# Kernel optimization log

Hardware: AMD Instinct MI355X
Metric: run time of the kernel (lower is better)

The kernel has to match this reference:

```python
import jax, jax.numpy as jnp
import numpy as np

B, N, KNN_K, T_FRAC = 8, 4096, 32, 0.5
C_IN, C_OUT = 4, 64


def _knn_group(q, db, kk):
    """q: [Nq,3] queries, db: [Nd,3] database. Returns feats [Nq,kk,4], nn [Nq,kk,3]."""
    d2 = (jnp.sum(q * q, axis=-1, keepdims=True)
          + jnp.sum(db * db, axis=-1)[None, :]
          - 2.0 * (q @ db.T))                      # [Nq,Nd] squared dists
    _, idx = jax.lax.top_k(-d2, kk)                 # ascending distance, like pytorch3d knn_points
    nn = db[idx]                                    # [Nq,kk,3]
    resi = nn - q[:, None, :]                       # [Nq,kk,3]
    sq = jnp.sum(resi * resi, axis=-1, keepdims=True)
    dist = jnp.where(sq > 0, jnp.sqrt(jnp.where(sq > 0, sq, 1.0)), 0.0)  # safe norm (exact fwd)
    feats = jnp.concatenate([resi, dist], axis=-1)  # [Nq,kk,4]
    return feats, nn


def _forward(points1, points2, pc, Wq, Wk, Wv, bq, bk, bv, ridx1, ridx2, k, t):
    k2 = int(k * t)
    k1 = k - k2
    p1 = jnp.swapaxes(points1, 1, 2)  # [B,N,3]
    p2 = jnp.swapaxes(points2, 1, 2)
    p3 = jnp.swapaxes(pc, 1, 2)

    def per_batch(a, b, c, i1, i2):
        newp = jnp.concatenate([a[i1], b[i2]], axis=0)     # [N,3] fused candidate set
        f1, g1 = _knn_group(newp, a, k1)
        f2, g2 = _knn_group(newp, b, k2)
        f3, g3 = _knn_group(newp, c, k)
        feats = jnp.concatenate([f1, f2, f3], axis=1)      # [N,2k,4]
        grouped = jnp.concatenate([g1, g2, g3], axis=1)    # [N,2k,3]
        return feats, grouped

    feats, grouped = jax.vmap(per_batch)(p1, p2, p3, ridx1, ridx2)  # [B,N,2k,4], [B,N,2k,3]

    # SelfAttention over the neighbor axis (per point group)
    q = feats @ Wq + bq          # [B,N,2k,C_OUT]
    kf = feats @ Wk + bk
    v = feats @ Wv + bv
    scale = 1.0 / np.sqrt(C_OUT).astype(np.float32)
    attn = jax.nn.softmax(jnp.einsum('bnkc,bnjc->bnkj', q, kf) * scale, axis=-1)
    y = jnp.einsum('bnkj,bnjc->bnkc', attn, v)             # [B,N,2k,C_OUT]

    score = jnp.max(y, axis=-1)                            # max over channels -> [B,N,2k]
    w = jax.nn.softmax(score, axis=-1)                     # weights over 2k neighbors
    fused = jnp.einsum('bnk,bnkd->bdn', w, grouped)        # [B,3,N]
    return fused


def setup_inputs() -> dict:
    key = jax.random.key(0)
    ks = jax.random.split(key, 8)
    points1 = jax.random.normal(ks[0], (B, 3, N), dtype=jnp.float32)
    points2 = jax.random.normal(ks[1], (B, 3, N), dtype=jnp.float32)
    pc = jax.random.normal(ks[2], (B, 3, N), dtype=jnp.float32)
    N2 = int(N * T_FRAC)
    N1 = N - N2
    perm = lambda kk: jax.random.permutation(kk, N)
    ridx1 = jax.vmap(perm)(jax.random.split(ks[3], B))[:, :N1].astype(jnp.int32)
    ridx2 = jax.vmap(perm)(jax.random.split(ks[4], B))[:, :N2].astype(jnp.int32)
    s = 1.0 / np.sqrt(C_IN)
    Wq = jax.random.normal(ks[5], (C_IN, C_OUT), dtype=jnp.float32) * s
    Wk = jax.random.normal(ks[6], (C_IN, C_OUT), dtype=jnp.float32) * s
    Wv = jax.random.normal(ks[7], (C_IN, C_OUT), dtype=jnp.float32) * s
    z = jnp.zeros((C_OUT,), dtype=jnp.float32)
    return {"points1": points1, "points2": points2, "pc": pc,
            "Wq": Wq, "Wk": Wk, "Wv": Wv, "bq": z, "bk": z, "bv": z,
            "ridx1": ridx1, "ridx2": ridx2, "k": KNN_K, "t": T_FRAC}


def reference(points1, points2, pc, Wq, Wk, Wv, bq, bk, bv, ridx1, ridx2, k, t):
    return _forward(points1, points2, pc, Wq, Wk, Wv, bq, bk, bv, ridx1, ridx2, k, t)
```

## Files before the change

kernel.cpp:

```cpp
#include <hip/hip_runtime.h>
#include <hip/hip_bf16.h>
#include <math.h>

#define NB   8
#define NPT  4096
#define NQ1  2048
#define NQ2  2048
#define KTOT 64
#define TILE 1024
#define NTHR 256
#define QPB  128
#define TBUF 16
#define MPAD 33

#define RCPLN2 1.4426950408889634f
#define EXP2F(x) __builtin_amdgcn_exp2f(x)

#define PRM_OFF  (4u << 20)
#define PACK_OFF ((4u << 20) + 4096)

__global__ __launch_bounds__(256) void pf2_pack(const float* __restrict__ p1,
                                                const float* __restrict__ p2,
                                                const float* __restrict__ pc,
                                                float4* __restrict__ packed) {
    int t = blockIdx.x * 256 + threadIdx.x;
    int b = t / (3 * NPT);
    int r = t - b * 3 * NPT;
    int db = r / NPT;
    int j = r - db * NPT;
    const float* src = (db == 0 ? p1 : db == 1 ? p2 : pc) + (size_t)b * 3 * NPT;
    packed[t] = make_float4(src[j], src[NPT + j], src[2 * NPT + j], 0.f);
}

__global__ void pf2_setup(const float* __restrict__ Wq, const float* __restrict__ Wk,
                          const float* __restrict__ bq, const float* __restrict__ bk,
                          float* __restrict__ prm) {
    int t = threadIdx.x;
    const float sc = 0.125f * RCPLN2;
    if (t < 16) {
        int p = t >> 2, q = t & 3;
        float a = 0.f;
        for (int c = 0; c < 64; ++c) a += Wq[p * 64 + c] * Wk[q * 64 + c];
        prm[t] = a * sc;
    } else if (t < 20) {
        int p = t - 16; float a = 0.f;
        for (int c = 0; c < 64; ++c) a += Wq[p * 64 + c] * bk[c];
        prm[t] = a * sc;
    } else if (t < 24) {
        int q = t - 20; float a = 0.f;
        for (int c = 0; c < 64; ++c) a += Wk[q * 64 + c] * bq[c];
        prm[t] = a * sc;
    } else if (t == 24) {
        float a = 0.f;
        for (int c = 0; c < 64; ++c) a += bq[c] * bk[c];
        prm[t] = a * sc;
    }
}

template <int K>
__device__ __forceinline__ void insert_med3(float (&dl)[K], int (&il)[K], float d, int id) {
    float pd = -INFINITY; int pi = 0;
    bool cp = false;
#pragma unroll
    for (int j = 0; j < K; ++j) {
        float oj = dl[j]; int ij = il[j];
        bool cj = d < oj;
        dl[j] = __builtin_amdgcn_fmed3f(d, pd, oj);
        il[j] = cp ? pi : (cj ? id : ij);
        pd = oj; pi = ij; cp = cj;
    }
}

template <int K>
__device__ void knn_half(const float* __restrict__ dbp,
                         float qx, float qy, float qz, int tid,
                         float4* __restrict__ tileLds,
                         unsigned short* __restrict__ bufLds,
                         float* __restrict__ mD,
                         unsigned short* __restrict__ mI,
                         unsigned short* __restrict__ outIdx) {
    const int q = tid & (QPB - 1), h = tid >> 7;
    float dl[K]; int il[K];
#pragma unroll
    for (int j = 0; j < K; ++j) { dl[j] = INFINITY; il[j] = 0; }
    float thresh = INFINITY;
    int cnt = 0;
    float4* tp = tileLds + h * TILE;

    for (int st = 0; st < 2; ++st) {
        int base = h * 2048 + st * TILE;
        __syncthreads();
        for (int r = 0; r < TILE / QPB; ++r) {
            int j = q + r * QPB;
            float x = dbp[base + j];
            float y = dbp[NPT + base + j];
            float z = dbp[2 * NPT + base + j];
            tp[j] = make_float4(-2.f * x, -2.f * y, -2.f * z,
                                fmaf(x, x, fmaf(y, y, z * z)));
        }
        __syncthreads();

        for (int c0 = 0; c0 < TILE; c0 += 8) {
            float sv[8];
#pragma unroll
            for (int u = 0; u < 8; ++u) {
                float4 p = tp[c0 + u];
                sv[u] = fmaf(p.x, qx, fmaf(p.y, qy, fmaf(p.z, qz, p.w)));
            }
#pragma unroll
            for (int u = 0; u < 8; ++u) {
                if (sv[u] < thresh) {
                    bufLds[cnt * NTHR + tid] = (unsigned short)(c0 + u);
                    ++cnt;
                }
            }
            if (__any(cnt > TBUF - 8)) {
                for (int u = 0; u < TBUF; ++u) {
                    if (!__any(u < cnt)) break;
                    bool act = (u < cnt);
                    int j = act ? bufLds[u * NTHR + tid] : 0;
                    float4 p = tp[j];
                    float s = fmaf(p.x, qx, fmaf(p.y, qy, fmaf(p.z, qz, p.w)));
                    bool pass = act && (s < dl[K - 1]);
                    if (__any(pass)) {
                        if (pass) insert_med3<K>(dl, il, s, base + j);
                    }
                }
                cnt = 0;
                thresh = dl[K - 1];
            }
        }
        for (int u = 0; u < TBUF; ++u) {
            if (!__any(u < cnt)) break;
            bool act = (u < cnt);
            int j = act ? bufLds[u * NTHR + tid] : 0;
            float4 p = tp[j];
            float s = fmaf(p.x, qx, fmaf(p.y, qy, fmaf(p.z, qz, p.w)));
            bool pass = act && (s < dl[K - 1]);
            if (__any(pass)) {
                if (pass) insert_med3<K>(dl, il, s, base + j);
            }
        }
        cnt = 0;
        thresh = dl[K - 1];
    }

    __syncthreads();
    if (h == 1) {
#pragma unroll
        for (int j = 0; j < K; ++j) {
            mD[q * MPAD + j] = dl[j];
            mI[q * MPAD + j] = (unsigned short)il[j];
        }
    }
    __syncthreads();
    if (h == 0) {
#pragma unroll
        for (int j = 0; j < K; ++j) {
            float d = mD[q * MPAD + j];
            int id = (int)mI[q * MPAD + j];
            if (d < dl[K - 1]) insert_med3<K>(dl, il, d, id);
        }
        unsigned* o32 = (unsigned*)outIdx;
#pragma unroll
        for (int u = 0; u < K / 2; ++u)
            o32[u] = (unsigned)(unsigned short)il[2 * u] |
                     ((unsigned)(unsigned short)il[2 * u + 1] << 16);
    }
}

__global__ __launch_bounds__(NTHR) void pf2_knn(const float* __restrict__ p1,
                                                const float* __restrict__ p2,
                                                const float* __restrict__ pc,
                                                const int* __restrict__ ridx1,
                                                const int* __restrict__ ridx2,
                                                unsigned short* __restrict__ wsIdx) {
    __shared__ float4 tileLds[2 * TILE];
    __shared__ unsigned short bufLds[TBUF * NTHR];
    float* mD = (float*)tileLds;
    unsigned short* mI = (unsigned short*)(mD + QPB * MPAD);

    int bid = blockIdx.x;
    int dbslot = bid >> 8;
    int db = (dbslot == 0) ? 2 : dbslot - 1;
    int rem = bid & 255;
    int b = rem >> 5;
    int chunk = rem & 31;
    int tid = threadIdx.x;
    int i = chunk * QPB + (tid & (QPB - 1));

    int j0; const float* srcp;
    if (i < NQ1) { j0 = ridx1[b * NQ1 + i]; srcp = p1; }
    else         { j0 = ridx2[b * NQ2 + (i - NQ1)]; srcp = p2; }
    const float* sb = srcp + (size_t)b * 3 * NPT;
    float qx = sb[j0], qy = sb[NPT + j0], qz = sb[2 * NPT + j0];

    const float* dbp = (db == 0 ? p1 : db == 1 ? p2 : pc) + (size_t)b * 3 * NPT;
    unsigned short* out = wsIdx + (size_t)(b * NPT + i) * KTOT +
                          (db == 0 ? 0 : db == 1 ? 16 : 32);
    if (db < 2) knn_half<16>(dbp, qx, qy, qz, tid, tileLds, bufLds, mD, mI, out);
    else        knn_half<32>(dbp, qx, qy, qz, tid, tileLds, bufLds, mD, mI, out);
}

__global__ __launch_bounds__(256) void pf2_attn(const float* __restrict__ p1,
                                                const float* __restrict__ p2,
                                                const float* __restrict__ pc,
                                                const int* __restrict__ ridx1,
                                                const int* __restrict__ ridx2,
                                                const float* __restrict__ Wv,
                                                const float* __restrict__ bv,
                                                const float* __restrict__ prm,
                                                const float4* __restrict__ packed,
                                                const unsigned short* __restrict__ wsIdx,
                                                float* __restrict__ out) {
    __shared__ float4 wvt[64];
    __shared__ float  bvs[64];
    __shared__ float  prms[25];
    __shared__ float4 gl[4][64];
    __shared__ float4 fl[4][64];
    __shared__ float  sl[4][64];

    int tid = threadIdx.x;
    if (tid < 64) {
        wvt[tid] = make_float4(Wv[tid], Wv[64 + tid], Wv[128 + tid], Wv[192 + tid]);
        bvs[tid] = bv[tid];
    } else if (tid < 89) {
        prms[tid - 64] = prm[tid - 64];
    }
    __syncthreads();

    int wv = tid >> 6, lane = tid & 63;
    int g = blockIdx.x * 4 + wv;
    int b = g >> 12;
    int i = g & 4095;

    int j0; const float* srcp;
    if (i < NQ1) { j0 = ridx1[b * NQ1 + i]; srcp = p1; }
    else         { j0 = ridx2[b * NQ2 + (i - NQ1)]; srcp = p2; }
    const float* sb = srcp + (size_t)b * 3 * NPT;
    float qx = sb[j0], qy = sb[NPT + j0], qz = sb[2 * NPT + j0];

    int nidx = (int)wsIdx[(size_t)(b * NPT + i) * KTOT + lane];
    int db = (lane < 16) ? 0 : (lane < 32) ? 1 : 2;
    float4 np = packed[(size_t)(b * 3 + db) * NPT + nidx];
    float nx = np.x, ny = np.y, nz = np.z;
    float fx = nx - qx, fy = ny - qy, fz = nz - qz;
    float sq = fx * fx + fy * fy + fz * fz;
    float fw = sq > 0.f ? sqrtf(sq) : 0.f;

    float gx = prms[0]  * fx + prms[1]  * fy + prms[2]  * fz + prms[3]  * fw;
    float gy = prms[4]  * fx + prms[5]  * fy + prms[6]  * fz + prms[7]  * fw;
    float gz = prms[8]  * fx + prms[9]  * fy + prms[10] * fz + prms[11] * fw;
    float gw = prms[12] * fx + prms[13] * fy + prms[14] * fz + prms[15] * fw;
    float sj = prms[20] * fx + prms[21] * fy + prms[22] * fz + prms[23] * fw;

    gl[wv][lane] = make_float4(gx, gy, gz, gw);
    fl[wv][lane] = make_float4(fx, fy, fz, fw);
    sl[wv][lane] = sj;
    __syncthreads();

    float m = -INFINITY;
    for (int j = 0; j < 64; ++j) {
        float4 gj = gl[wv][j];
        float l = fx * gj.x + fy * gj.y + fz * gj.z + fw * gj.w + sl[wv][j];
        m = fmaxf(m, l);
    }
    float S = 0.f, H0 = 0.f, H1 = 0.f, H2 = 0.f, H3 = 0.f;
    for (int j = 0; j < 64; ++j) {
        float4 gj = gl[wv][j];
        float4 fj = fl[wv][j];
        float l = fx * gj.x + fy * gj.y + fz * gj.z + fw * gj.w + sl[wv][j];
        float e = EXP2F(l - m);
        S += e;
        H0 += e * fj.x; H1 += e * fj.y; H2 += e * fj.z; H3 += e * fj.w;
    }
    float rS = 1.f / S;

    float smax = -INFINITY;
    for (int ch = 0; ch < 64; ++ch) {
        float4 wc = wvt[ch];
        float t = H0 * wc.x + H1 * wc.y + H2 * wc.z + H3 * wc.w;
        float yv = fmaf(t, rS, bvs[ch]);
        smax = fmaxf(smax, yv);
    }

    float M = smax;
    for (int off = 32; off; off >>= 1) M = fmaxf(M, __shfl_xor(M, off));
    float e = EXP2F((smax - M) * RCPLN2);
    float E = e;
    for (int off = 32; off; off >>= 1) E += __shfl_xor(E, off);
    float w = e / E;
    float px = w * nx, py = w * ny, pz = w * nz;
    for (int off = 32; off; off >>= 1) {
        px += __shfl_xor(px, off);
        py += __shfl_xor(py, off);
        pz += __shfl_xor(pz, off);
    }
    if (lane == 0) {
        float* ob = out + (size_t)b * 3 * NPT + i;
        ob[0] = px; ob[NPT] = py; ob[2 * NPT] = pz;
    }
}

extern "C" void kernel_launch(void* const* d_in, const int* in_sizes, int n_in,
                              void* d_out, int out_size, void* d_ws, size_t ws_size,
                              hipStream_t stream) {
    const float* p1 = (const float*)d_in[0];
    const float* p2 = (const float*)d_in[1];
    const float* pc = (const float*)d_in[2];
    const float* Wq = (const float*)d_in[3];
    const float* Wk = (const float*)d_in[4];
    const float* Wv = (const float*)d_in[5];
    const float* bq = (const float*)d_in[6];
    const float* bk = (const float*)d_in[7];
    const float* bv = (const float*)d_in[8];
    const int* ridx1 = (const int*)d_in[9];
    const int* ridx2 = (const int*)d_in[10];
    float* out = (float*)d_out;

    unsigned short* wsIdx = (unsigned short*)d_ws;
    float* prm = (float*)((char*)d_ws + PRM_OFF);
    float4* packed = (float4*)((char*)d_ws + PACK_OFF);

    pf2_pack<<<(3 * NB * NPT) / 256, 256, 0, stream>>>(p1, p2, pc, packed);
    pf2_setup<<<1, 32, 0, stream>>>(Wq, Wk, bq, bk, prm);
    pf2_knn<<<NB * 3 * (NPT / QPB), NTHR, 0, stream>>>(p1, p2, pc, ridx1, ridx2, wsIdx);
    pf2_attn<<<NB * NPT / 4, 256, 0, stream>>>(p1, p2, pc, ridx1, ridx2, Wv, bv, prm,
                                               packed, wsIdx, out);
}
```

Baseline: 378.4 us.

## Two-pass KNN: distance-only top-K threshold then index selection over full LDS tile

The KNN selection is split into two passes. The first keeps only sorted distances, buffering raw distance values so candidates need no recompute and no index bookkeeping, and yields the exact K-th distance. The second rescans with that threshold and inserts indices for only the few survivors. The whole 4096-point database is now staged once into LDS (64KB tile, larger buffer of 32-bit entries), which removes the per-subtile reload syncs but doubles the distance computation and raises LDS use, which may lower occupancy.

```diff
diff --git a/kernel.cpp b/kernel.cpp
--- a/kernel.cpp
+++ b/kernel.cpp
@@ -7,7 +7,6 @@
 #define NQ1  2048
 #define NQ2  2048
 #define KTOT 64
-#define TILE 1024
 #define NTHR 256
 #define QPB  128
 #define TBUF 16
@@ -72,84 +71,100 @@
 }
 
 template <int K>
-__device__ void knn_half(const float* __restrict__ dbp,
-                         float qx, float qy, float qz, int tid,
-                         float4* __restrict__ tileLds,
-                         unsigned short* __restrict__ bufLds,
+__device__ void knn_half(float qx, float qy, float qz, int tid,
+                         const float4* __restrict__ tile,
+                         unsigned* __restrict__ dbuf,
                          float* __restrict__ mD,
                          unsigned short* __restrict__ mI,
                          unsigned short* __restrict__ outIdx) {
     const int q = tid & (QPB - 1), h = tid >> 7;
-    float dl[K]; int il[K];
-#pragma unroll
-    for (int j = 0; j < K; ++j) { dl[j] = INFINITY; il[j] = 0; }
+    const int base = h * 2048;
+
+    float dl[K];
+#pragma unroll
+    for (int j = 0; j < K; ++j) dl[j] = INFINITY;
     float thresh = INFINITY;
     int cnt = 0;
-    float4* tp = tileLds + h * TILE;
-
-    for (int st = 0; st < 2; ++st) {
-        int base = h * 2048 + st * TILE;
-        __syncthreads();
-        for (int r = 0; r < TILE / QPB; ++r) {
-            int j = q + r * QPB;
-            float x = dbp[base + j];
-            float y = dbp[NPT + base + j];
-            float z = dbp[2 * NPT + base + j];
-            tp[j] = make_float4(-2.f * x, -2.f * y, -2.f * z,
-                                fmaf(x, x, fmaf(y, y, z * z)));
-        }
-        __syncthreads();
-
-        for (int c0 = 0; c0 < TILE; c0 += 8) {
-            float sv[8];
-#pragma unroll
-            for (int u = 0; u < 8; ++u) {
-                float4 p = tp[c0 + u];
-                sv[u] = fmaf(p.x, qx, fmaf(p.y, qy, fmaf(p.z, qz, p.w)));
+
+    auto flushD = [&]() {
+        for (int u = 0; u < TBUF; ++u) {
+            if (!__any(u < cnt)) break;
+            unsigned bits = dbuf[u * NTHR + tid];
+            float s = (u < cnt) ? __uint_as_float(bits) : INFINITY;
+            float pd = -INFINITY;
+#pragma unroll
+            for (int j = 0; j < K; ++j) {
+                float oj = dl[j];
+                dl[j] = __builtin_amdgcn_fmed3f(s, pd, oj);
+                pd = oj;
             }
-#pragma unroll
-            for (int u = 0; u < 8; ++u) {
-                if (sv[u] < thresh) {
-                    bufLds[cnt * NTHR + tid] = (unsigned short)(c0 + u);
-                    ++cnt;
-                }
+        }
+        cnt = 0;
+        thresh = dl[K - 1];
+    };
+
+    for (int c0 = 0; c0 < 2048; c0 += 8) {
+        float sv[8];
+#pragma unroll
+        for (int u = 0; u < 8; ++u) {
+            float4 p = tile[base + c0 + u];
+            sv[u] = fmaf(p.x, qx, fmaf(p.y, qy, fmaf(p.z, qz, p.w)));
+        }
+#pragma unroll
+        for (int u = 0; u < 8; ++u) {
+            if (sv[u] < thresh) {
+                dbuf[cnt * NTHR + tid] = __float_as_uint(sv[u]);
+                ++cnt;
             }
-            if (__any(cnt > TBUF - 8)) {
-                for (int u = 0; u < TBUF; ++u) {
-                    if (!__any(u < cnt)) break;
-                    bool act = (u < cnt);
-                    int j = act ? bufLds[u * NTHR + tid] : 0;
-                    float4 p = tp[j];
-                    float s = fmaf(p.x, qx, fmaf(p.y, qy, fmaf(p.z, qz, p.w)));
-                    bool pass = act && (s < dl[K - 1]);
-                    if (__any(pass)) {
-                        if (pass) insert_med3<K>(dl, il, s, base + j);
-                    }
-                }
-                cnt = 0;
-                thresh = dl[K - 1];
-            }
-        }
+        }
+        if (__any(cnt > TBUF - 8)) flushD();
+    }
+    flushD();
+    const float mt = dl[K - 1];
+
+    int il[K]; float dl2[K];
+#pragma unroll
+    for (int j = 0; j < K; ++j) { dl2[j] = INFINITY; il[j] = 0; }
+    cnt = 0;
+
+    auto flushI = [&]() {
         for (int u = 0; u < TBUF; ++u) {
             if (!__any(u < cnt)) break;
             bool act = (u < cnt);
-            int j = act ? bufLds[u * NTHR + tid] : 0;
-            float4 p = tp[j];
+            int idx = act ? (int)dbuf[u * NTHR + tid] : 0;
+            float4 p = tile[idx];
             float s = fmaf(p.x, qx, fmaf(p.y, qy, fmaf(p.z, qz, p.w)));
-            bool pass = act && (s < dl[K - 1]);
+            bool pass = act && (s < dl2[K - 1]);
             if (__any(pass)) {
-                if (pass) insert_med3<K>(dl, il, s, base + j);
+                if (pass) insert_med3<K>(dl2, il, s, idx);
             }
         }
         cnt = 0;
-        thresh = dl[K - 1];
-    }
+    };
+
+    for (int c0 = 0; c0 < 2048; c0 += 8) {
+        float sv[8];
+#pragma unroll
+        for (int u = 0; u < 8; ++u) {
+            float4 p = tile[base + c0 + u];
+            sv[u] = fmaf(p.x, qx, fmaf(p.y, qy, fmaf(p.z, qz, p.w)));
+        }
+#pragma unroll
+        for (int u = 0; u < 8; ++u) {
+            if (sv[u] <= mt) {
+                dbuf[cnt * NTHR + tid] = (unsigned)(base + c0 + u);
+                ++cnt;
+            }
+        }
+        if (__any(cnt > TBUF - 8)) flushI();
+    }
+    flushI();
 
     __syncthreads();
     if (h == 1) {
 #pragma unroll
         for (int j = 0; j < K; ++j) {
-            mD[q * MPAD + j] = dl[j];
+            mD[q * MPAD + j] = dl2[j];
             mI[q * MPAD + j] = (unsigned short)il[j];
         }
     }
@@ -159,7 +174,7 @@
         for (int j = 0; j < K; ++j) {
             float d = mD[q * MPAD + j];
             int id = (int)mI[q * MPAD + j];
-            if (d < dl[K - 1]) insert_med3<K>(dl, il, d, id);
+            if (d < dl2[K - 1]) insert_med3<K>(dl2, il, d, id);
         }
         unsigned* o32 = (unsigned*)outIdx;
 #pragma unroll
@@ -175,8 +190,8 @@
                                                 const int* __restrict__ ridx1,
                                                 const int* __restrict__ ridx2,
                                                 unsigned short* __restrict__ wsIdx) {
-    __shared__ float4 tileLds[2 * TILE];
-    __shared__ unsigned short bufLds[TBUF * NTHR];
+    __shared__ float4 tileLds[NPT];
+    __shared__ unsigned dbuf[TBUF * NTHR];
     float* mD = (float*)tileLds;
     unsigned short* mI = (unsigned short*)(mD + QPB * MPAD);
 
@@ -196,10 +211,21 @@
     float qx = sb[j0], qy = sb[NPT + j0], qz = sb[2 * NPT + j0];
 
     const float* dbp = (db == 0 ? p1 : db == 1 ? p2 : pc) + (size_t)b * 3 * NPT;
+
+    for (int r = 0; r < NPT / NTHR; ++r) {
+        int j = tid + r * NTHR;
+        float x = dbp[j];
+        float y = dbp[NPT + j];
+        float z = dbp[2 * NPT + j];
+        tileLds[j] = make_float4(-2.f * x, -2.f * y, -2.f * z,
+                                 fmaf(x, x, fmaf(y, y, z * z)));
+    }
+    __syncthreads();
+
     unsigned short* out = wsIdx + (size_t)(b * NPT + i) * KTOT +
                           (db == 0 ? 0 : db == 1 ? 16 : 32);
-    if (db < 2) knn_half<16>(dbp, qx, qy, qz, tid, tileLds, bufLds, mD, mI, out);
-    else        knn_half<32>(dbp, qx, qy, qz, tid, tileLds, bufLds, mD, mI, out);
+    if (db < 2) knn_half<16>(qx, qy, qz, tid, tileLds, dbuf, mD, mI, out);
+    else        knn_half<32>(qx, qy, qz, tid, tileLds, dbuf, mD, mI, out);
 }
 
 __global__ __launch_bounds__(256) void pf2_attn(const float* __restrict__ p1,
```

Measured after the change: 543.0 us. 1.44x slower.
